# Kernel optimization log

Measured on AMD Instinct MI355X. Metric: run time of the kernel, lower is better.

The kernel has to match this reference:

```python
import jax, jax.numpy as jnp
import numpy as np

# ---- static config (from search_space / module defaults) ----
B, NCG = 4096, 2                 # batch of archs, cell groups
NUM_INIT, NUM_NODE_INPUTS, NUM_STEPS = 2, 2, 4
NUM_NODES = NUM_INIT + NUM_STEPS  # 6
N_EDGE = NUM_NODE_INPUTS * NUM_STEPS  # 8
NUM_OPS = 7                      # 'none' is index 0
NONE_INDEX = 0
NODE_DIM = OP_DIM = HIDDEN = 48
GCN_DIMS = [128, 128]


def _uniform(key, shape, fan_in):
    s = 1.0 / np.sqrt(fan_in)
    return jax.random.uniform(key, shape, minval=-s, maxval=s, dtype=jnp.float32)


def setup_inputs() -> dict:
    key = jax.random.key(0)
    ks = jax.random.split(key, 14)
    # from-node for step i must be < NUM_INIT + i -> per-edge maxval [2,2,3,3,4,4,5,5]
    fmax = jnp.repeat(jnp.arange(NUM_INIT, NUM_NODES), NUM_NODE_INPUTS)
    f_nodes = jax.random.randint(ks[0], (B, NCG, N_EDGE), 0, fmax)
    ops = jax.random.randint(ks[1], (B, NCG, N_EDGE), 0, NUM_OPS)
    archs = jnp.stack([f_nodes, ops], axis=2).astype(jnp.int32)  # (B,NCG,2,E)

    init_node_emb = jax.random.normal(ks[2], (NCG, NUM_INIT, NODE_DIM), dtype=jnp.float32)
    other_node_emb = jnp.zeros((NCG, 1, NODE_DIM), dtype=jnp.float32)  # zero-init, trainable
    # op embeddings; 'none' op (idx 0) is frozen zeros
    op_embs = jax.random.normal(ks[3], (NUM_OPS, OP_DIM), dtype=jnp.float32).at[NONE_INDEX].set(0.0)

    Wx = _uniform(ks[4], (NODE_DIM, HIDDEN), NODE_DIM)
    bx = _uniform(ks[5], (HIDDEN,), NODE_DIM)
    W1 = _uniform(ks[6], (HIDDEN, GCN_DIMS[0]), GCN_DIMS[0])
    Wa1 = _uniform(ks[7], (OP_DIM, GCN_DIMS[0]), OP_DIM)
    ba1 = _uniform(ks[8], (GCN_DIMS[0],), OP_DIM)
    W2 = _uniform(ks[9], (GCN_DIMS[0], GCN_DIMS[1]), GCN_DIMS[1])
    Wa2 = _uniform(ks[10], (OP_DIM, GCN_DIMS[1]), OP_DIM)
    ba2 = _uniform(ks[11], (GCN_DIMS[1],), OP_DIM)
    return {"archs": archs, "init_node_emb": init_node_emb, "other_node_emb": other_node_emb,
            "op_embs": op_embs, "Wx": Wx, "bx": bx, "W1": W1, "Wa1": Wa1, "ba1": ba1,
            "W2": W2, "Wa2": Wa2, "ba2": ba2}


def _build_adj_ops(archs):
    """Dense adjacency (edge counts) and per-input-slot op-index matrices."""
    f = archs[:, :, 0, :].reshape(-1, N_EDGE)    # (B*NCG, E) from-nodes
    ops = archs[:, :, 1, :].reshape(-1, N_EDGE)  # (B*NCG, E) op ids
    t = jnp.repeat(jnp.arange(NUM_INIT, NUM_NODES), NUM_NODE_INPUTS)  # (E,) to-nodes
    Bt = B * NCG
    b_idx = jnp.arange(Bt)[:, None]
    adj = jnp.zeros((Bt, NUM_NODES, NUM_NODES), jnp.float32)
    adj = adj.at[b_idx, t[None, :], f].add(1.0)
    adj_op_inds = []
    for k in range(NUM_NODE_INPUTS):
        fk, tk, opk = f[:, k::NUM_NODE_INPUTS], t[k::NUM_NODE_INPUTS], ops[:, k::NUM_NODE_INPUTS]
        aoi = jnp.full((Bt, NUM_NODES, NUM_NODES), NONE_INDEX, dtype=jnp.int32)
        aoi = aoi.at[b_idx, tk[None, :], fk].set(opk)  # (t,f) unique within a slot
        adj_op_inds.append(aoi.reshape(B, NCG, NUM_NODES, NUM_NODES))
    return adj.reshape(B, NCG, NUM_NODES, NUM_NODES), adj_op_inds


def _gcn_layer(y, adj_op_inds, op_embs, W, Wa, ba):
    """DenseGraphOpEdgeFlow (defaults: attention, no plus_I/normalize/bias):
    out_i = support_i + sum_slots sum_j sigmoid(att(op_emb[op_ij])) * 1[op_ij != none] * support_j
    """
    support = y @ W                                   # (B,CG,N,out)
    out = support
    for aoi in adj_op_inds:
        attn = jax.nn.sigmoid(op_embs[aoi] @ Wa + ba)  # (B,CG,N,N,out)
        attn = attn * (aoi != NONE_INDEX)[..., None].astype(support.dtype)
        out = out + jnp.einsum('bcijo,bcjo->bcio', attn, support)
    return out


def reference(archs, init_node_emb, other_node_emb, op_embs, Wx, bx,
              W1, Wa1, ba1, W2, Wa2, ba2):
    _adj, adj_op_inds = _build_adj_ops(archs)  # adj counts unused under default gcn_kwargs
    node = jnp.concatenate([
        jnp.broadcast_to(init_node_emb[None], (B, NCG, NUM_INIT, NODE_DIM)),
        jnp.broadcast_to(other_node_emb[None], (B, NCG, NUM_STEPS, NODE_DIM))], axis=2)
    y = node @ Wx + bx                                 # x_hidden
    y = _gcn_layer(y, adj_op_inds, op_embs, W1, Wa1, ba1)
    y = jax.nn.relu(y)                                 # relu between layers
    y = _gcn_layer(y, adj_op_inds, op_embs, W2, Wa2, ba2)
    y = y[:, :, NUM_INIT:, :].mean(axis=2)             # drop init nodes, mean over steps
    return y.reshape(B, -1)                            # (B, NCG*128)
```

## Files before the change

### kernel.cpp

```cpp
#include <hip/hip_runtime.h>

#define NPAIR 8192

#define NCFG_REAL 5292
#define NCFG      5296
#define CPER      2646
#define WS_AT2F   0
#define WS_TAB    1024
#define WS_NEED   ((size_t)(1024 + NCFG * 128) * 4)

#define COMP4(v, j) ((j) == 0 ? (v).x : (j) == 1 ? (v).y : (j) == 2 ? (v).z : (v).w)

__device__ __forceinline__ float sigmoidf_(float x) {
  return 1.0f / (1.0f + __expf(-x));
}

__global__ __launch_bounds__(512) void config_kernel(
    const float* __restrict__ init_emb, const float* __restrict__ other_emb,
    const float* __restrict__ op_embs,  const float* __restrict__ Wx,
    const float* __restrict__ bx,       const float* __restrict__ W1,
    const float* __restrict__ Wa1,      const float* __restrict__ ba1,
    const float* __restrict__ W2,       const float* __restrict__ Wa2,
    const float* __restrict__ ba2,      float* __restrict__ ws)
{
  __shared__ __align__(16) float wsh[8192];
  __shared__ __align__(16) float s1sh[1536];
  __shared__ __align__(16) float at1sh[896];
  __shared__ __align__(16) float at2sh[896];
  __shared__ __align__(16) float y0[576];
  const int t = threadIdx.x;

  for (int i = t; i < 576; i += 512) ((float4*)wsh)[i] = ((const float4*)Wx)[i];
  if (t < 48)       ((float4*)at2sh)[t] = ((const float4*)init_emb)[t];
  else if (t < 72)  ((float4*)at2sh)[t] = ((const float4*)other_emb)[t - 48];
  else if (t < 84)  ((float4*)at2sh)[t] = ((const float4*)bx)[t - 72];
  __syncthreads();

  for (int idx = t; idx < 576; idx += 512) {
    int c = idx / 288, i = (idx / 48) % 6, h = idx % 48;
    const float* nptr = (i < 2) ? (at2sh + (c * 2 + i) * 48)
                                : (at2sh + 192 + c * 48);
    float acc = at2sh[288 + h];
    for (int d = 0; d < 48; ++d) acc += nptr[d] * wsh[d * 48 + h];
    y0[idx] = acc;
  }
  __syncthreads();

  for (int i = t; i < 1536; i += 512) ((float4*)wsh)[i] = ((const float4*)W1)[i];
  __syncthreads();
  for (int idx = t; idx < 1536; idx += 512) {
    int ci = idx >> 7, o = idx & 127;
    const float* yp = y0 + ci * 48;
    float acc = 0.f;
    for (int h = 0; h < 48; ++h) acc += yp[h] * wsh[h * 128 + o];
    s1sh[idx] = acc;
  }
  __syncthreads();

  for (int i = t; i < 1536; i += 512) ((float4*)wsh)[i] = ((const float4*)Wa1)[i];
  if (t < 84) ((float4*)y0)[t] = ((const float4*)op_embs)[t];
  __syncthreads();
  for (int idx = t; idx < 896; idx += 512) {
    int op = idx >> 7, o = idx & 127;
    float a = ba1[o];
    for (int d = 0; d < 48; ++d) a += y0[op * 48 + d] * wsh[d * 128 + o];
    at1sh[idx] = a;
  }
  __syncthreads();

  for (int i = t; i < 1536; i += 512) ((float4*)wsh)[i] = ((const float4*)Wa2)[i];
  __syncthreads();
  for (int idx = t; idx < 896; idx += 512) {
    int op = idx >> 7, o = idx & 127;
    float a2 = ba2[o];
    for (int d = 0; d < 48; ++d) a2 += y0[op * 48 + d] * wsh[d * 128 + o];
    float v1 = (op == 0) ? 0.f : sigmoidf_(at1sh[idx]);
    float v2 = (op == 0) ? 0.f : sigmoidf_(a2);
    at1sh[idx] = v1;
    at2sh[idx] = v2;
    ws[WS_AT2F + idx] = v2;
  }
  __syncthreads();

  const int w  = t >> 6, o2 = t & 63;
  const int cfg0 = (blockIdx.x * 8 + w) * 8;
  const float2* s1f = (const float2*)s1sh;
  const float2* a1f = (const float2*)at1sh;

  #pragma unroll
  for (int r = 0; r < 8; ++r) {
    int cfg = cfg0 + r;
    if (cfg >= NCFG) continue;
    float2 v;
    if (cfg < NCFG_REAL) {
      int c = cfg / CPER, q = cfg % CPER;
      int i, b;
      if (q < 196)       { i = 2; b = 0; }
      else if (q < 637)  { i = 3; b = 196; }
      else if (q < 1421) { i = 4; b = 637; }
      else               { i = 5; b = 1421; }
      q -= b;
      int op2_ = q % 7; q /= 7;
      int f2_  = q % i; q /= i;
      int op1_ = q % 7;
      int f1_  = q / 7;
      int cb = c * 384;
      v = s1f[cb + i * 64 + o2];
      float2 A0 = a1f[op1_ * 64 + o2], B0 = s1f[cb + f1_ * 64 + o2];
      float2 A1 = a1f[op2_ * 64 + o2], B1 = s1f[cb + f2_ * 64 + o2];
      v.x += A0.x * B0.x + A1.x * B1.x;
      v.y += A0.y * B0.y + A1.y * B1.y;
    } else {
      int j = cfg - NCFG_REAL, c = j >> 1, i = j & 1;
      v = s1f[c * 384 + i * 64 + o2];
    }
    ((float2*)(wsh + (w * 8 + r) * 128))[o2] =
        make_float2(fmaxf(v.x, 0.f), fmaxf(v.y, 0.f));
  }
  __syncthreads();

  const float* yb = wsh + (w * 8) * 128;
  const float2* W2f = (const float2*)W2;
  float2 acc[8];
  #pragma unroll
  for (int r = 0; r < 8; ++r) acc[r] = make_float2(0.f, 0.f);

  for (int k = 0; k < 128; k += 4) {
    float4 yv[8];
    #pragma unroll
    for (int r = 0; r < 8; ++r)
      yv[r] = *(const float4*)(yb + r * 128 + k);
    #pragma unroll
    for (int j = 0; j < 4; ++j) {
      float2 wv = W2f[(k + j) * 64 + o2];
      #pragma unroll
      for (int r = 0; r < 8; ++r) {
        float y = COMP4(yv[r], j);
        acc[r].x += y * wv.x;
        acc[r].y += y * wv.y;
      }
    }
  }

  float2* tab = (float2*)(ws + WS_TAB);
  #pragma unroll
  for (int r = 0; r < 8; ++r) {
    int cfg = cfg0 + r;
    if (cfg < NCFG) tab[cfg * 64 + o2] = acc[r];
  }
}

__global__ __launch_bounds__(256) void gather_kernel(
    const int* __restrict__ archs, const float* __restrict__ ws,
    float* __restrict__ out)
{
  const int t  = threadIdx.x;
  const int pp = t >> 6;
  const int o2 = t & 63;
  const int P  = blockIdx.x * 4 + pp;
  const int c  = P & 1;

  __shared__ int archsh[64];
  if (t < 64) archsh[t] = archs[blockIdx.x * 64 + t];
  __syncthreads();

  int f[8], op[8];
  #pragma unroll
  for (int e = 0; e < 8; ++e) { f[e] = archsh[pp * 16 + e]; op[e] = archsh[pp * 16 + 8 + e]; }

  const float2* tab = (const float2*)(ws + WS_TAB);
  const float2* a2f = (const float2*)(ws + WS_AT2F);

  float2 S0 = tab[(NCFG_REAL + c * 2 + 0) * 64 + o2];
  float2 S1 = tab[(NCFG_REAL + c * 2 + 1) * 64 + o2];
  float2 S2, S3, S4, S5;
  {
    const int ib[4] = {0, 196, 637, 1421};
    #pragma unroll
    for (int i = 2; i < 6; ++i) {
      int e0 = 2 * (i - 2), e1 = e0 + 1;
      int cid = c * CPER + ib[i - 2] +
                ((f[e0] * 7 + op[e0]) * i + f[e1]) * 7 + op[e1];
      float2 v = tab[cid * 64 + o2];
      if (i == 2) S2 = v; else if (i == 3) S3 = v;
      else if (i == 4) S4 = v; else S5 = v;
    }
  }
  float2 A2[8];
  #pragma unroll
  for (int e = 0; e < 8; ++e) A2[e] = a2f[op[e] * 64 + o2];

  float r0 = S2.x + S3.x + S4.x + S5.x;
  float r1 = S2.y + S3.y + S4.y + S5.y;
  #pragma unroll
  for (int e = 0; e < 8; ++e) {
    int fe = f[e];
    float sx, sy;
    if (fe == 0)      { sx = S0.x; sy = S0.y; }
    else if (fe == 1) { sx = S1.x; sy = S1.y; }
    else if (fe == 2) { sx = S2.x; sy = S2.y; }
    else if (fe == 3) { sx = S3.x; sy = S3.y; }
    else              { sx = S4.x; sy = S4.y; }
    r0 += A2[e].x * sx;
    r1 += A2[e].y * sy;
  }
  ((float2*)out)[P * 64 + o2] = make_float2(r0 * 0.25f, r1 * 0.25f);
}

#define FB_S1   0
#define FB_AT1  1536
#define FB_AT2  2432
#define FB_S2I  3328

__global__ __launch_bounds__(512) void precompute_kernel(
    const float* __restrict__ init_emb, const float* __restrict__ other_emb,
    const float* __restrict__ op_embs,  const float* __restrict__ Wx,
    const float* __restrict__ bx,       const float* __restrict__ W1,
    const float* __restrict__ Wa1,      const float* __restrict__ ba1,
    const float* __restrict__ W2,       const float* __restrict__ Wa2,
    const float* __restrict__ ba2,      float* __restrict__ ws)
{
  const int t   = threadIdx.x;
  const int blk = blockIdx.x;
  __shared__ float y0[576];
  __shared__ float s1sh[1536];
  for (int idx = t; idx < 576; idx += 512) {
    int c = idx / 288, i = (idx / 48) % 6, h = idx % 48;
    const float* nptr = (i < 2) ? (init_emb + (c * 2 + i) * 48)
                                : (other_emb + c * 48);
    float acc = bx[h];
    for (int d = 0; d < 48; ++d) acc += nptr[d] * Wx[d * 48 + h];
    y0[idx] = acc;
  }
  __syncthreads();
  for (int idx = t; idx < 1536; idx += 512) {
    int ci = idx >> 7, o = idx & 127;
    const float* yp = y0 + ci * 48;
    float acc = 0.f;
    for (int h = 0; h < 48; ++h) acc += yp[h] * W1[h * 128 + o];
    s1sh[idx] = acc;
    ws[FB_S1 + idx] = acc;
  }
  for (int idx = blk * 112 + t; idx < (blk + 1) * 112; idx += 512) {
    int op = idx >> 7, o = idx & 127;
    float a1 = ba1[o], a2 = ba2[o];
    for (int d = 0; d < 48; ++d) {
      float e = op_embs[op * 48 + d];
      a1 += e * Wa1[d * 128 + o];
      a2 += e * Wa2[d * 128 + o];
    }
    ws[FB_AT1 + idx] = (op == 0) ? 0.f : sigmoidf_(a1);
    ws[FB_AT2 + idx] = (op == 0) ? 0.f : sigmoidf_(a2);
  }
  __syncthreads();
  for (int idx = blk * 64 + t; idx < (blk + 1) * 64; idx += 512) {
    int c = idx >> 8, i = (idx >> 7) & 1, o = idx & 127;
    const float* sp = s1sh + (c * 6 + i) * 128;
    float acc = 0.f;
    for (int h = 0; h < 128; ++h) acc += fmaxf(sp[h], 0.f) * W2[h * 128 + o];
    ws[FB_S2I + idx] = acc;
  }
}

__global__ __launch_bounds__(256) void main_kernel(
    const int* __restrict__ archs, const float* __restrict__ W2,
    const float* __restrict__ ws, float* __restrict__ out)
{
  const int t  = threadIdx.x;
  const int pp = t >> 6;
  const int o2 = t & 63;
  const int P  = blockIdx.x * 4 + pp;
  const int c  = P & 1;
  __shared__ float y1sh[4][512];
  __shared__ int   archsh[64];
  if (t < 64) archsh[t] = archs[blockIdx.x * 64 + t];
  __syncthreads();
  int f[8], op[8];
  #pragma unroll
  for (int e = 0; e < 8; ++e) { f[e] = archsh[pp * 16 + e]; op[e] = archsh[pp * 16 + 8 + e]; }
  const float2* s1p = (const float2*)ws + c * 384;
  const float2* at1 = (const float2*)(ws + FB_AT1);
  const float2* at2 = (const float2*)(ws + FB_AT2);
  const float2* s2i = (const float2*)(ws + FB_S2I) + c * 128;
  float2 A2[8];
  #pragma unroll
  for (int e = 0; e < 8; ++e) A2[e] = at2[op[e] * 64 + o2];
  float2 S0 = s2i[o2], S1 = s2i[64 + o2];
  #pragma unroll
  for (int i = 0; i < 4; ++i) {
    float2 v = s1p[(2 + i) * 64 + o2];
    int e0 = 2 * i, e1 = 2 * i + 1;
    float2 A0 = at1[op[e0] * 64 + o2];
    float2 B0 = s1p[f[e0] * 64 + o2];
    float2 A1 = at1[op[e1] * 64 + o2];
    float2 B1 = s1p[f[e1] * 64 + o2];
    v.x += A0.x * B0.x + A1.x * B1.x;
    v.y += A0.y * B0.y + A1.y * B1.y;
    ((float2*)(y1sh[pp] + i * 128))[o2] =
        make_float2(fmaxf(v.x, 0.f), fmaxf(v.y, 0.f));
  }
  __syncthreads();
  const float* y1p = y1sh[pp];
  const float2* W2f = (const float2*)W2;
  float ax0 = 0, ax1 = 0, ax2 = 0, ax3 = 0;
  float ay0 = 0, ay1 = 0, ay2 = 0, ay3 = 0;
  for (int h = 0; h < 128; h += 4) {
    float4 q0 = *(const float4*)(y1p + 0 * 128 + h);
    float4 q1 = *(const float4*)(y1p + 1 * 128 + h);
    float4 q2 = *(const float4*)(y1p + 2 * 128 + h);
    float4 q3 = *(const float4*)(y1p + 3 * 128 + h);
    #pragma unroll
    for (int j = 0; j < 4; ++j) {
      float2 wf = W2f[(h + j) * 64 + o2];
      float w0 = wf.x, w1 = wf.y, y;
      y = COMP4(q0, j); ax0 += y * w0; ay0 += y * w1;
      y = COMP4(q1, j); ax1 += y * w0; ay1 += y * w1;
      y = COMP4(q2, j); ax2 += y * w0; ay2 += y * w1;
      y = COMP4(q3, j); ax3 += y * w0; ay3 += y * w1;
    }
  }
  float r0 = ax0 + ax1 + ax2 + ax3;
  float r1 = ay0 + ay1 + ay2 + ay3;
  #pragma unroll
  for (int e = 0; e < 8; ++e) {
    int fe = f[e];
    float sx, sy;
    if (fe == 0)      { sx = S0.x; sy = S0.y; }
    else if (fe == 1) { sx = S1.x; sy = S1.y; }
    else if (fe == 2) { sx = ax0; sy = ay0; }
    else if (fe == 3) { sx = ax1; sy = ay1; }
    else if (fe == 4) { sx = ax2; sy = ay2; }
    else              { sx = ax3; sy = ay3; }
    r0 += A2[e].x * sx;
    r1 += A2[e].y * sy;
  }
  ((float2*)out)[P * 64 + o2] = make_float2(r0 * 0.25f, r1 * 0.25f);
}

extern "C" void kernel_launch(void* const* d_in, const int* in_sizes, int n_in,
                              void* d_out, int out_size, void* d_ws, size_t ws_size,
                              hipStream_t stream) {
  const int* archs = (const int*)d_in[0];
  float* ws = (float*)d_ws;
  if (ws_size >= WS_NEED) {
    config_kernel<<<83, 512, 0, stream>>>(
        (const float*)d_in[1], (const float*)d_in[2], (const float*)d_in[3],
        (const float*)d_in[4], (const float*)d_in[5], (const float*)d_in[6],
        (const float*)d_in[7], (const float*)d_in[8], (const float*)d_in[9],
        (const float*)d_in[10], (const float*)d_in[11], ws);
    gather_kernel<<<NPAIR / 4, 256, 0, stream>>>(archs, ws, (float*)d_out);
  } else {
    precompute_kernel<<<8, 512, 0, stream>>>(
        (const float*)d_in[1], (const float*)d_in[2], (const float*)d_in[3],
        (const float*)d_in[4], (const float*)d_in[5], (const float*)d_in[6],
        (const float*)d_in[7], (const float*)d_in[8], (const float*)d_in[9],
        (const float*)d_in[10], (const float*)d_in[11], ws);
    main_kernel<<<NPAIR / 4, 256, 0, stream>>>(archs, (const float*)d_in[9], ws,
                                               (float*)d_out);
  }
}
```

Baseline: 103.6 us.

## Fuse config-table build and gather into one cooperative kernel with grid sync

After: 275.2 us. 2.66x slower.

```diff
diff --git a/kernel.cpp b/kernel.cpp
--- a/kernel.cpp
+++ b/kernel.cpp
@@ -1,4 +1,7 @@
 #include <hip/hip_runtime.h>
+#include <hip/hip_cooperative_groups.h>
+
+namespace cg = cooperative_groups;
 
 #define NPAIR 8192
 
@@ -15,21 +18,15 @@
   return 1.0f / (1.0f + __expf(-x));
 }
 
-__global__ __launch_bounds__(512) void config_kernel(
+__device__ __forceinline__ void build_tables(
     const float* __restrict__ init_emb, const float* __restrict__ other_emb,
     const float* __restrict__ op_embs,  const float* __restrict__ Wx,
     const float* __restrict__ bx,       const float* __restrict__ W1,
     const float* __restrict__ Wa1,      const float* __restrict__ ba1,
-    const float* __restrict__ W2,       const float* __restrict__ Wa2,
-    const float* __restrict__ ba2,      float* __restrict__ ws)
-{
-  __shared__ __align__(16) float wsh[8192];
-  __shared__ __align__(16) float s1sh[1536];
-  __shared__ __align__(16) float at1sh[896];
-  __shared__ __align__(16) float at2sh[896];
-  __shared__ __align__(16) float y0[576];
-  const int t = threadIdx.x;
-
+    const float* __restrict__ Wa2,      const float* __restrict__ ba2,
+    float* __restrict__ ws,
+    float* wsh, float* s1sh, float* at1sh, float* at2sh, float* y0, int t)
+{
   for (int i = t; i < 576; i += 512) ((float4*)wsh)[i] = ((const float4*)Wx)[i];
   if (t < 48)       ((float4*)at2sh)[t] = ((const float4*)init_emb)[t];
   else if (t < 72)  ((float4*)at2sh)[t] = ((const float4*)other_emb)[t - 48];
@@ -81,6 +78,169 @@
     ws[WS_AT2F + idx] = v2;
   }
   __syncthreads();
+}
+
+__device__ __forceinline__ void gather_pair(
+    const int* __restrict__ archs, const float* __restrict__ ws,
+    float* __restrict__ out, int P, int o2)
+{
+  const int c = P & 1;
+  const int* ap = archs + P * 16;
+  int f[8], op[8];
+  #pragma unroll
+  for (int e = 0; e < 8; ++e) { f[e] = ap[e]; op[e] = ap[8 + e]; }
+
+  const float2* tab = (const float2*)(ws + WS_TAB);
+  const float2* a2f = (const float2*)(ws + WS_AT2F);
+
+  float2 S0 = tab[(NCFG_REAL + c * 2 + 0) * 64 + o2];
+  float2 S1 = tab[(NCFG_REAL + c * 2 + 1) * 64 + o2];
+  float2 S2, S3, S4, S5;
+  {
+    const int ib[4] = {0, 196, 637, 1421};
+    #pragma unroll
+    for (int i = 2; i < 6; ++i) {
+      int e0 = 2 * (i - 2), e1 = e0 + 1;
+      int cid = c * CPER + ib[i - 2] +
+                ((f[e0] * 7 + op[e0]) * i + f[e1]) * 7 + op[e1];
+      float2 v = tab[cid * 64 + o2];
+      if (i == 2) S2 = v; else if (i == 3) S3 = v;
+      else if (i == 4) S4 = v; else S5 = v;
+    }
+  }
+  float2 A2[8];
+  #pragma unroll
+  for (int e = 0; e < 8; ++e) A2[e] = a2f[op[e] * 64 + o2];
+
+  float r0 = S2.x + S3.x + S4.x + S5.x;
+  float r1 = S2.y + S3.y + S4.y + S5.y;
+  #pragma unroll
+  for (int e = 0; e < 8; ++e) {
+    int fe = f[e];
+    float sx, sy;
+    if (fe == 0)      { sx = S0.x; sy = S0.y; }
+    else if (fe == 1) { sx = S1.x; sy = S1.y; }
+    else if (fe == 2) { sx = S2.x; sy = S2.y; }
+    else if (fe == 3) { sx = S3.x; sy = S3.y; }
+    else              { sx = S4.x; sy = S4.y; }
+    r0 += A2[e].x * sx;
+    r1 += A2[e].y * sy;
+  }
+  ((float2*)out)[P * 64 + o2] = make_float2(r0 * 0.25f, r1 * 0.25f);
+}
+
+__global__ __launch_bounds__(512) void coop_kernel(
+    const int*   __restrict__ archs,
+    const float* __restrict__ init_emb, const float* __restrict__ other_emb,
+    const float* __restrict__ op_embs,  const float* __restrict__ Wx,
+    const float* __restrict__ bx,       const float* __restrict__ W1,
+    const float* __restrict__ Wa1,      const float* __restrict__ ba1,
+    const float* __restrict__ W2,       const float* __restrict__ Wa2,
+    const float* __restrict__ ba2,      float* __restrict__ ws,
+    float* __restrict__ out)
+{
+  __shared__ __align__(16) float wsh[8192];
+  __shared__ __align__(16) float s1sh[1536];
+  __shared__ __align__(16) float at1sh[896];
+  __shared__ __align__(16) float at2sh[896];
+  __shared__ __align__(16) float y0[576];
+  const int t = threadIdx.x;
+
+  build_tables(init_emb, other_emb, op_embs, Wx, bx, W1, Wa1, ba1, Wa2, ba2,
+               ws, wsh, s1sh, at1sh, at2sh, y0, t);
+
+  const int w  = t >> 6, o2 = t & 63;
+  const int wid  = blockIdx.x * 8 + w;
+  const int cfg0 = wid * 3;
+  const float2* s1f = (const float2*)s1sh;
+  const float2* a1f = (const float2*)at1sh;
+
+  #pragma unroll
+  for (int r = 0; r < 3; ++r) {
+    int cfg = cfg0 + r;
+    float2 v = make_float2(0.f, 0.f);
+    if (cfg < NCFG_REAL) {
+      int c = cfg / CPER, q = cfg % CPER;
+      int i, b;
+      if (q < 196)       { i = 2; b = 0; }
+      else if (q < 637)  { i = 3; b = 196; }
+      else if (q < 1421) { i = 4; b = 637; }
+      else               { i = 5; b = 1421; }
+      q -= b;
+      int op2_ = q % 7; q /= 7;
+      int f2_  = q % i; q /= i;
+      int op1_ = q % 7;
+      int f1_  = q / 7;
+      int cb = c * 384;
+      v = s1f[cb + i * 64 + o2];
+      float2 A0 = a1f[op1_ * 64 + o2], B0 = s1f[cb + f1_ * 64 + o2];
+      float2 A1 = a1f[op2_ * 64 + o2], B1 = s1f[cb + f2_ * 64 + o2];
+      v.x += A0.x * B0.x + A1.x * B1.x;
+      v.y += A0.y * B0.y + A1.y * B1.y;
+    } else if (cfg < NCFG) {
+      int j = cfg - NCFG_REAL, c = j >> 1, i = j & 1;
+      v = s1f[c * 384 + i * 64 + o2];
+    }
+    ((float2*)(wsh + (w * 3 + r) * 128))[o2] =
+        make_float2(fmaxf(v.x, 0.f), fmaxf(v.y, 0.f));
+  }
+  __syncthreads();
+
+  const float* yb = wsh + (w * 3) * 128;
+  const float2* W2f = (const float2*)W2;
+  float2 acc[3];
+  #pragma unroll
+  for (int r = 0; r < 3; ++r) acc[r] = make_float2(0.f, 0.f);
+
+  for (int k = 0; k < 128; k += 4) {
+    float4 yv[3];
+    #pragma unroll
+    for (int r = 0; r < 3; ++r)
+      yv[r] = *(const float4*)(yb + r * 128 + k);
+    #pragma unroll
+    for (int j = 0; j < 4; ++j) {
+      float2 wv = W2f[(k + j) * 64 + o2];
+      #pragma unroll
+      for (int r = 0; r < 3; ++r) {
+        float y = COMP4(yv[r], j);
+        acc[r].x += y * wv.x;
+        acc[r].y += y * wv.y;
+      }
+    }
+  }
+  float2* tab = (float2*)(ws + WS_TAB);
+  #pragma unroll
+  for (int r = 0; r < 3; ++r) {
+    int cfg = cfg0 + r;
+    if (cfg < NCFG) tab[cfg * 64 + o2] = acc[r];
+  }
+
+  cg::this_grid().sync();
+
+  #pragma unroll
+  for (int k = 0; k < 4; ++k) {
+    int P = blockIdx.x * 32 + w * 4 + k;
+    gather_pair(archs, ws, out, P, o2);
+  }
+}
+
+__global__ __launch_bounds__(512) void config_kernel(
+    const float* __restrict__ init_emb, const float* __restrict__ other_emb,
+    const float* __restrict__ op_embs,  const float* __restrict__ Wx,
+    const float* __restrict__ bx,       const float* __restrict__ W1,
+    const float* __restrict__ Wa1,      const float* __restrict__ ba1,
+    const float* __restrict__ W2,       const float* __restrict__ Wa2,
+    const float* __restrict__ ba2,      float* __restrict__ ws)
+{
+  __shared__ __align__(16) float wsh[8192];
+  __shared__ __align__(16) float s1sh[1536];
+  __shared__ __align__(16) float at1sh[896];
+  __shared__ __align__(16) float at2sh[896];
+  __shared__ __align__(16) float y0[576];
+  const int t = threadIdx.x;
+
+  build_tables(init_emb, other_emb, op_embs, Wx, bx, W1, Wa1, ba1, Wa2, ba2,
+               ws, wsh, s1sh, at1sh, at2sh, y0, t);
 
   const int w  = t >> 6, o2 = t & 63;
   const int cfg0 = (blockIdx.x * 8 + w) * 8;
@@ -124,7 +284,6 @@
   float2 acc[8];
   #pragma unroll
   for (int r = 0; r < 8; ++r) acc[r] = make_float2(0.f, 0.f);
-
   for (int k = 0; k < 128; k += 4) {
     float4 yv[8];
     #pragma unroll
@@ -141,7 +300,6 @@
       }
     }
   }
-
   float2* tab = (float2*)(ws + WS_TAB);
   #pragma unroll
   for (int r = 0; r < 8; ++r) {
@@ -158,204 +316,37 @@
   const int pp = t >> 6;
   const int o2 = t & 63;
   const int P  = blockIdx.x * 4 + pp;
-  const int c  = P & 1;
-
-  __shared__ int archsh[64];
-  if (t < 64) archsh[t] = archs[blockIdx.x * 64 + t];
-  __syncthreads();
-
-  int f[8], op[8];
-  #pragma unroll
-  for (int e = 0; e < 8; ++e) { f[e] = archsh[pp * 16 + e]; op[e] = archsh[pp * 16 + 8 + e]; }
-
-  const float2* tab = (const float2*)(ws + WS_TAB);
-  const float2* a2f = (const float2*)(ws + WS_AT2F);
-
-  float2 S0 = tab[(NCFG_REAL + c * 2 + 0) * 64 + o2];
-  float2 S1 = tab[(NCFG_REAL + c * 2 + 1) * 64 + o2];
-  float2 S2, S3, S4, S5;
-  {
-    const int ib[4] = {0, 196, 637, 1421};
-    #pragma unroll
-    for (int i = 2; i < 6; ++i) {
-      int e0 = 2 * (i - 2), e1 = e0 + 1;
-      int cid = c * CPER + ib[i - 2] +
-                ((f[e0] * 7 + op[e0]) * i + f[e1]) * 7 + op[e1];
-      float2 v = tab[cid * 64 + o2];
-      if (i == 2) S2 = v; else if (i == 3) S3 = v;
-      else if (i == 4) S4 = v; else S5 = v;
-    }
-  }
-  float2 A2[8];
-  #pragma unroll
-  for (int e = 0; e < 8; ++e) A2[e] = a2f[op[e] * 64 + o2];
-
-  float r0 = S2.x + S3.x + S4.x + S5.x;
-  float r1 = S2.y + S3.y + S4.y + S5.y;
-  #pragma unroll
-  for (int e = 0; e < 8; ++e) {
-    int fe = f[e];
-    float sx, sy;
-    if (fe == 0)      { sx = S0.x; sy = S0.y; }
-    else if (fe == 1) { sx = S1.x; sy = S1.y; }
-    else if (fe == 2) { sx = S2.x; sy = S2.y; }
-    else if (fe == 3) { sx = S3.x; sy = S3.y; }
-    else              { sx = S4.x; sy = S4.y; }
-    r0 += A2[e].x * sx;
-    r1 += A2[e].y * sy;
-  }
-  ((float2*)out)[P * 64 + o2] = make_float2(r0 * 0.25f, r1 * 0.25f);
-}
-
-#define FB_S1   0
-#define FB_AT1  1536
-#define FB_AT2  2432
-#define FB_S2I  3328
-
-__global__ __launch_bounds__(512) void precompute_kernel(
-    const float* __restrict__ init_emb, const float* __restrict__ other_emb,
-    const float* __restrict__ op_embs,  const float* __restrict__ Wx,
-    const float* __restrict__ bx,       const float* __restrict__ W1,
-    const float* __restrict__ Wa1,      const float* __restrict__ ba1,
-    const float* __restrict__ W2,       const float* __restrict__ Wa2,
-    const float* __restrict__ ba2,      float* __restrict__ ws)
-{
-  const int t   = threadIdx.x;
-  const int blk = blockIdx.x;
-  __shared__ float y0[576];
-  __shared__ float s1sh[1536];
-  for (int idx = t; idx < 576; idx += 512) {
-    int c = idx / 288, i = (idx / 48) % 6, h = idx % 48;
-    const float* nptr = (i < 2) ? (init_emb + (c * 2 + i) * 48)
-                                : (other_emb + c * 48);
-    float acc = bx[h];
-    for (int d = 0; d < 48; ++d) acc += nptr[d] * Wx[d * 48 + h];
-    y0[idx] = acc;
-  }
-  __syncthreads();
-  for (int idx = t; idx < 1536; idx += 512) {
-    int ci = idx >> 7, o = idx & 127;
-    const float* yp = y0 + ci * 48;
-    float acc = 0.f;
-    for (int h = 0; h < 48; ++h) acc += yp[h] * W1[h * 128 + o];
-    s1sh[idx] = acc;
-    ws[FB_S1 + idx] = acc;
-  }
-  for (int idx = blk * 112 + t; idx < (blk + 1) * 112; idx += 512) {
-    int op = idx >> 7, o = idx & 127;
-    float a1 = ba1[o], a2 = ba2[o];
-    for (int d = 0; d < 48; ++d) {
-      float e = op_embs[op * 48 + d];
-      a1 += e * Wa1[d * 128 + o];
-      a2 += e * Wa2[d * 128 + o];
-    }
-    ws[FB_AT1 + idx] = (op == 0) ? 0.f : sigmoidf_(a1);
-    ws[FB_AT2 + idx] = (op == 0) ? 0.f : sigmoidf_(a2);
-  }
-  __syncthreads();
-  for (int idx = blk * 64 + t; idx < (blk + 1) * 64; idx += 512) {
-    int c = idx >> 8, i = (idx >> 7) & 1, o = idx & 127;
-    const float* sp = s1sh + (c * 6 + i) * 128;
-    float acc = 0.f;
-    for (int h = 0; h < 128; ++h) acc += fmaxf(sp[h], 0.f) * W2[h * 128 + o];
-    ws[FB_S2I + idx] = acc;
-  }
-}
-
-__global__ __launch_bounds__(256) void main_kernel(
-    const int* __restrict__ archs, const float* __restrict__ W2,
-    const float* __restrict__ ws, float* __restrict__ out)
-{
-  const int t  = threadIdx.x;
-  const int pp = t >> 6;
-  const int o2 = t & 63;
-  const int P  = blockIdx.x * 4 + pp;
-  const int c  = P & 1;
-  __shared__ float y1sh[4][512];
-  __shared__ int   archsh[64];
-  if (t < 64) archsh[t] = archs[blockIdx.x * 64 + t];
-  __syncthreads();
-  int f[8], op[8];
-  #pragma unroll
-  for (int e = 0; e < 8; ++e) { f[e] = archsh[pp * 16 + e]; op[e] = archsh[pp * 16 + 8 + e]; }
-  const float2* s1p = (const float2*)ws + c * 384;
-  const float2* at1 = (const float2*)(ws + FB_AT1);
-  const float2* at2 = (const float2*)(ws + FB_AT2);
-  const float2* s2i = (const float2*)(ws + FB_S2I) + c * 128;
-  float2 A2[8];
-  #pragma unroll
-  for (int e = 0; e < 8; ++e) A2[e] = at2[op[e] * 64 + o2];
-  float2 S0 = s2i[o2], S1 = s2i[64 + o2];
-  #pragma unroll
-  for (int i = 0; i < 4; ++i) {
-    float2 v = s1p[(2 + i) * 64 + o2];
-    int e0 = 2 * i, e1 = 2 * i + 1;
-    float2 A0 = at1[op[e0] * 64 + o2];
-    float2 B0 = s1p[f[e0] * 64 + o2];
-    float2 A1 = at1[op[e1] * 64 + o2];
-    float2 B1 = s1p[f[e1] * 64 + o2];
-    v.x += A0.x * B0.x + A1.x * B1.x;
-    v.y += A0.y * B0.y + A1.y * B1.y;
-    ((float2*)(y1sh[pp] + i * 128))[o2] =
-        make_float2(fmaxf(v.x, 0.f), fmaxf(v.y, 0.f));
-  }
-  __syncthreads();
-  const float* y1p = y1sh[pp];
-  const float2* W2f = (const float2*)W2;
-  float ax0 = 0, ax1 = 0, ax2 = 0, ax3 = 0;
-  float ay0 = 0, ay1 = 0, ay2 = 0, ay3 = 0;
-  for (int h = 0; h < 128; h += 4) {
-    float4 q0 = *(const float4*)(y1p + 0 * 128 + h);
-    float4 q1 = *(const float4*)(y1p + 1 * 128 + h);
-    float4 q2 = *(const float4*)(y1p + 2 * 128 + h);
-    float4 q3 = *(const float4*)(y1p + 3 * 128 + h);
-    #pragma unroll
-    for (int j = 0; j < 4; ++j) {
-      float2 wf = W2f[(h + j) * 64 + o2];
-      float w0 = wf.x, w1 = wf.y, y;
-      y = COMP4(q0, j); ax0 += y * w0; ay0 += y * w1;
-      y = COMP4(q1, j); ax1 += y * w0; ay1 += y * w1;
-      y = COMP4(q2, j); ax2 += y * w0; ay2 += y * w1;
-      y = COMP4(q3, j); ax3 += y * w0; ay3 += y * w1;
-    }
-  }
-  float r0 = ax0 + ax1 + ax2 + ax3;
-  float r1 = ay0 + ay1 + ay2 + ay3;
-  #pragma unroll
-  for (int e = 0; e < 8; ++e) {
-    int fe = f[e];
-    float sx, sy;
-    if (fe == 0)      { sx = S0.x; sy = S0.y; }
-    else if (fe == 1) { sx = S1.x; sy = S1.y; }
-    else if (fe == 2) { sx = ax0; sy = ay0; }
-    else if (fe == 3) { sx = ax1; sy = ay1; }
-    else if (fe == 4) { sx = ax2; sy = ay2; }
-    else              { sx = ax3; sy = ay3; }
-    r0 += A2[e].x * sx;
-    r1 += A2[e].y * sy;
-  }
-  ((float2*)out)[P * 64 + o2] = make_float2(r0 * 0.25f, r1 * 0.25f);
+  gather_pair(archs, ws, out, P, o2);
 }
 
 extern "C" void kernel_launch(void* const* d_in, const int* in_sizes, int n_in,
                               void* d_out, int out_size, void* d_ws, size_t ws_size,
                               hipStream_t stream) {
-  const int* archs = (const int*)d_in[0];
-  float* ws = (float*)d_ws;
-  if (ws_size >= WS_NEED) {
+  const int*   archs    = (const int*)d_in[0];
+  const float* init_emb = (const float*)d_in[1];
+  const float* other_e  = (const float*)d_in[2];
+  const float* op_embs  = (const float*)d_in[3];
+  const float* Wx       = (const float*)d_in[4];
+  const float* bx       = (const float*)d_in[5];
+  const float* W1       = (const float*)d_in[6];
+  const float* Wa1      = (const float*)d_in[7];
+  const float* ba1      = (const float*)d_in[8];
+  const float* W2       = (const float*)d_in[9];
+  const float* Wa2      = (const float*)d_in[10];
+  const float* ba2      = (const float*)d_in[11];
+  float* ws   = (float*)d_ws;
+  float* outp = (float*)d_out;
+
+  void* args[] = {
+    (void*)&archs, (void*)&init_emb, (void*)&other_e, (void*)&op_embs,
+    (void*)&Wx, (void*)&bx, (void*)&W1, (void*)&Wa1, (void*)&ba1,
+    (void*)&W2, (void*)&Wa2, (void*)&ba2, (void*)&ws, (void*)&outp
+  };
+  hipError_t err = hipLaunchCooperativeKernel(
+      reinterpret_cast<void*>(coop_kernel), dim3(256), dim3(512), args, 0, stream);
+  if (err != hipSuccess) {
     config_kernel<<<83, 512, 0, stream>>>(
-        (const float*)d_in[1], (const float*)d_in[2], (const float*)d_in[3],
-        (const float*)d_in[4], (const float*)d_in[5], (const float*)d_in[6],
-        (const float*)d_in[7], (const float*)d_in[8], (const float*)d_in[9],
-        (const float*)d_in[10], (const float*)d_in[11], ws);
-    gather_kernel<<<NPAIR / 4, 256, 0, stream>>>(archs, ws, (float*)d_out);
-  } else {
-    precompute_kernel<<<8, 512, 0, stream>>>(
-        (const float*)d_in[1], (const float*)d_in[2], (const float*)d_in[3],
-        (const float*)d_in[4], (const float*)d_in[5], (const float*)d_in[6],
-        (const float*)d_in[7], (const float*)d_in[8], (const float*)d_in[9],
-        (const float*)d_in[10], (const float*)d_in[11], ws);
-    main_kernel<<<NPAIR / 4, 256, 0, stream>>>(archs, (const float*)d_in[9], ws,
-                                               (float*)d_out);
-  }
-}
+        init_emb, other_e, op_embs, Wx, bx, W1, Wa1, ba1, W2, Wa2, ba2, ws);
+    gather_kernel<<<NPAIR / 4, 256, 0, stream>>>(archs, ws, outp);
+  }
+}
```
